# Kernel tuning notes

Measured on AMD Instinct MI355X. Metric: run time of the kernel, lower is better.

The kernel has to match this reference:

```python
import jax, jax.numpy as jnp
import numpy as np

SHARED_DIM = 512
ENC_IN = 512
LATENT = 16
BATCH = 65536
NUM_CLASSES = 16


def setup_inputs() -> dict:
    key = jax.random.key(0)
    ks = jax.random.split(key, 12)
    s = 1.0 / np.sqrt(SHARED_DIM)
    si = 1.0 / np.sqrt(ENC_IN)
    return {
        "x": jax.random.normal(ks[0], (BATCH, ENC_IN), dtype=jnp.float32),
        # shared MLP: two ReLU hiddens + identity output (rlkit Mlp)
        "W0": jax.random.uniform(ks[1], (SHARED_DIM, ENC_IN), jnp.float32, -si, si),
        "b0": jnp.zeros((SHARED_DIM,), jnp.float32),
        "W1": jax.random.uniform(ks[2], (SHARED_DIM, SHARED_DIM), jnp.float32, -s, s),
        "b1": jnp.zeros((SHARED_DIM,), jnp.float32),
        "W2": jax.random.uniform(ks[3], (SHARED_DIM, SHARED_DIM), jnp.float32, -s, s),
        "b2": jnp.zeros((SHARED_DIM,), jnp.float32),
        # class encoder (router)
        "Wc": jax.random.uniform(ks[4], (NUM_CLASSES, SHARED_DIM), jnp.float32, -s, s),
        "bc": jnp.zeros((NUM_CLASSES,), jnp.float32),
        # per-class gaussian experts, stacked: [K, 2*latent, shared_dim]
        "Wg": jax.random.uniform(ks[5], (NUM_CLASSES, 2 * LATENT, SHARED_DIM), jnp.float32, -s, s),
        "bg": jnp.zeros((NUM_CLASSES, 2 * LATENT), jnp.float32),
    }


def reference(x, W0, b0, W1, b1, W2, b2, Wc, bc, Wg, bg):
    # shared encoder: ReLU MLP with identity output layer
    m = jax.nn.relu(x @ W0.T + b0)
    m = jax.nn.relu(m @ W1.T + b1)
    m = m @ W2.T + b2                      # [B, D]
    # router: softmax over classes, then most-likely class per sample
    y_probs = jax.nn.softmax(m @ Wc.T + bc, axis=-1)   # [B, K]
    y = jnp.argmax(y_probs, axis=1)                    # [B]
    # evaluate ALL per-class experts densely (as the original does)
    mu_sigma = jnp.einsum('bd,ked->bke', m, Wg) + bg   # [B, K, 2L]
    mu = mu_sigma[..., :LATENT]                        # Normal mean; sampler='mean'
    # gather the selected class's mean per sample
    z = jnp.take_along_axis(mu, y[:, None, None], axis=1)[:, 0, :]  # [B, L]
    return (z, y)
```

## Files before the change

### kernel.cpp

```cpp
#include <hip/hip_runtime.h>
#include <hip/hip_bf16.h>

typedef __attribute__((ext_vector_type(8))) short short8;
typedef __attribute__((ext_vector_type(16))) float floatx16;
typedef __attribute__((ext_vector_type(4))) float floatx4;

#define AS1 __attribute__((address_space(1)))
#define AS3 __attribute__((address_space(3)))

constexpr int MM = 65536;
constexpr int KK = 512;
constexpr int NN = 512;

#define GK 32
#define LDT 40

__device__ __forceinline__ unsigned short bf16_rn(float v) {
  unsigned u = __float_as_uint(v);
  return (unsigned short)((u + 0x7FFFu + ((u >> 16) & 1u)) >> 16);
}
__device__ __forceinline__ float bf16_to_f32(unsigned short h) {
  return __uint_as_float((unsigned)h << 16);
}

__global__ __launch_bounds__(256) void split_kernel(
    const float* __restrict__ src, unsigned short* __restrict__ h,
    unsigned short* __restrict__ l, int n4) {
  int i = blockIdx.x * 256 + threadIdx.x;
  if (i >= n4) return;
  float4 v = ((const float4*)src)[i];
  ushort4 hv, lv;
  hv.x = bf16_rn(v.x); lv.x = bf16_rn(v.x - bf16_to_f32(hv.x));
  hv.y = bf16_rn(v.y); lv.y = bf16_rn(v.y - bf16_to_f32(hv.y));
  hv.z = bf16_rn(v.z); lv.z = bf16_rn(v.z - bf16_to_f32(hv.z));
  hv.w = bf16_rn(v.w); lv.w = bf16_rn(v.w - bf16_to_f32(hv.w));
  ((ushort4*)h)[i] = hv;
  ((ushort4*)l)[i] = lv;
}

template<bool RELU>
__global__ __launch_bounds__(512, 1) void gemm_mfma(
    const unsigned short* __restrict__ Ah, const unsigned short* __restrict__ Al,
    const unsigned short* __restrict__ Wh, const unsigned short* __restrict__ Wl,
    const float* __restrict__ bias,
    unsigned short* __restrict__ Ch, unsigned short* __restrict__ Cl) {
  __shared__ __align__(16) unsigned short smem[65536];
  const int tid = threadIdx.x;
  const int lane = tid & 63;
  const int wid = tid >> 6;
  const int wr = wid >> 2;
  const int wc = wid & 3;
  const int nwg = gridDim.x;
  const int hw  = blockIdx.x;
  const int logical = (hw & 7) * (nwg >> 3) + (hw >> 3);
  const int bm = logical >> 1, bn = logical & 1;
  const size_t Abase = (size_t)bm * 256 * KK;
  const size_t Bbase = (size_t)bn * 256 * KK;

  const int sarr  = wid >> 1;
  const int rbase = (wid & 1) * 128;
  const unsigned short* gsrc = (sarr == 0) ? Ah : (sarr == 1) ? Al
                             : (sarr == 2) ? Wh : Wl;
  const size_t tb = (sarr < 2) ? Abase : Bbase;
  const int rowl = lane >> 2;
  const int gch  = (lane & 3) ^ ((lane >> 3) & 3);
  const unsigned short* gbase = gsrc + tb + (size_t)(rbase + rowl) * KK + gch * 8;
  unsigned short* ldst = smem + sarr * 8192 + rbase * 32;

  auto stage2 = [&](int buf, int kk, int p) {
#pragma unroll
    for (int j = p * 2; j < p * 2 + 2; ++j) {
      __builtin_amdgcn_global_load_lds(
          (const AS1 unsigned int*)(gbase + (size_t)(j * 16) * KK + kk),
          (AS3 unsigned int*)(ldst + buf * 32768 + j * 16 * 32),
          16, 0, 0);
    }
  };

  floatx16 acc[4][2];
#pragma unroll
  for (int i = 0; i < 4; ++i)
#pragma unroll
    for (int j = 0; j < 2; ++j)
#pragma unroll
      for (int r = 0; r < 16; ++r) acc[i][j][r] = 0.f;

#pragma unroll
  for (int p = 0; p < 4; ++p) stage2(0, 0, p);

  const int swz = (lane >> 1) & 3;
#pragma unroll
  for (int t = 0; t < 16; ++t) {
    const int cur = t & 1;
    const unsigned short* base = smem + cur * 32768;
    short8 fbh[2], fbl[2];
#pragma unroll
    for (int p = 0; p < 4; ++p) {
      const int ks = p >> 1, h = p & 1;
      const int ch = ks * 2 + (lane >> 5);
      const int sw = (ch ^ swz) * 8;
      short8 fah[2], fal[2];

      if (p == 0) {
        if (t < 15) {
          stage2(cur ^ 1, (t + 1) * GK, 0);
          asm volatile("s_waitcnt vmcnt(2)" ::: "memory");
        } else {
          asm volatile("s_waitcnt vmcnt(0)" ::: "memory");
        }
        __builtin_amdgcn_s_barrier();
        __builtin_amdgcn_sched_barrier(0);
      }

#pragma unroll
      for (int q = 0; q < 2; ++q) {
        int row = wr * 128 + (h * 2 + q) * 32 + (lane & 31);
        fah[q] = *(const short8*)(base + row * 32 + sw);
        fal[q] = *(const short8*)(base + 8192 + row * 32 + sw);
      }
      if (h == 0) {
#pragma unroll
        for (int si = 0; si < 2; ++si) {
          int col = wc * 64 + si * 32 + (lane & 31);
          fbh[si] = *(const short8*)(base + 16384 + col * 32 + sw);
          fbl[si] = *(const short8*)(base + 24576 + col * 32 + sw);
        }
      }

      if (p > 0) {
        if (t < 15) stage2(cur ^ 1, (t + 1) * GK, p);
        __builtin_amdgcn_sched_barrier(0);
        __builtin_amdgcn_s_barrier();
        __builtin_amdgcn_sched_barrier(0);
      }

      __builtin_amdgcn_s_setprio(1);
#pragma unroll
      for (int q = 0; q < 2; ++q)
#pragma unroll
        for (int si = 0; si < 2; ++si) {
          const int ri = h * 2 + q;
          acc[ri][si] = __builtin_amdgcn_mfma_f32_32x32x16_bf16(fah[q], fbh[si], acc[ri][si], 0, 0, 0);
          acc[ri][si] = __builtin_amdgcn_mfma_f32_32x32x16_bf16(fah[q], fbl[si], acc[ri][si], 0, 0, 0);
          acc[ri][si] = __builtin_amdgcn_mfma_f32_32x32x16_bf16(fal[q], fbh[si], acc[ri][si], 0, 0, 0);
        }
      __builtin_amdgcn_s_setprio(0);
      __builtin_amdgcn_sched_barrier(0);
      __builtin_amdgcn_s_barrier();
    }
  }

  float bv[2];
#pragma unroll
  for (int si = 0; si < 2; ++si)
    bv[si] = bias[bn * 256 + wc * 64 + si * 32 + (lane & 31)];

  unsigned* lds32 = (unsigned*)smem;
#pragma unroll
  for (int ri = 0; ri < 4; ++ri) {
    __syncthreads();
#pragma unroll
    for (int si = 0; si < 2; ++si) {
      int lcol = wc * 64 + si * 32 + (lane & 31);
#pragma unroll
      for (int r = 0; r < 16; ++r) {
        int frow = (r & 3) + 8 * (r >> 2) + 4 * (lane >> 5);
        float v = acc[ri][si][r] + bv[si];
        if (RELU) v = fmaxf(v, 0.f);
        unsigned short h = bf16_rn(v);
        unsigned short lo = bf16_rn(v - bf16_to_f32(h));
        lds32[(wr * 32 + frow) * 256 + lcol] = (unsigned)h | ((unsigned)lo << 16);
      }
    }
    __syncthreads();
#pragma unroll
    for (int p = 0; p < 8; ++p) {
      int c = tid + p * 512;
      int lrow = c >> 6;
      int cc = (c & 63) * 4;
      uint4 d = *(const uint4*)&lds32[lrow * 256 + cc];
      ushort4 hv, lv;
      hv.x = (unsigned short)(d.x); lv.x = (unsigned short)(d.x >> 16);
      hv.y = (unsigned short)(d.y); lv.y = (unsigned short)(d.y >> 16);
      hv.z = (unsigned short)(d.z); lv.z = (unsigned short)(d.z >> 16);
      hv.w = (unsigned short)(d.w); lv.w = (unsigned short)(d.w >> 16);
      int grow = bm * 256 + (lrow >> 5) * 128 + ri * 32 + (lrow & 31);
      size_t gi = (size_t)grow * NN + bn * 256 + cc;
      *(ushort4*)&Ch[gi] = hv;
      *(ushort4*)&Cl[gi] = lv;
    }
  }
}

__global__ __launch_bounds__(512, 1) void gemm_x(
    const float* __restrict__ X,
    const unsigned short* __restrict__ Wh, const unsigned short* __restrict__ Wl,
    const float* __restrict__ bias,
    unsigned short* __restrict__ Ch, unsigned short* __restrict__ Cl) {
  __shared__ __align__(16) unsigned short smem[65536];
  const int tid = threadIdx.x;
  const int lane = tid & 63;
  const int wid = tid >> 6;
  const int wr = wid >> 2;
  const int wc = wid & 3;
  const int nwg = gridDim.x;
  const int hw  = blockIdx.x;
  const int logical = (hw & 7) * (nwg >> 3) + (hw >> 3);
  const int bm = logical >> 1, bn = logical & 1;

  const int barr = wid >> 2;
  const int brb  = (wid & 3) * 64;
  const int rowl = lane >> 2;
  const int gch  = (lane & 3) ^ ((lane >> 3) & 3);
  const unsigned short* gbB = (barr ? Wl : Wh) + (size_t)bn * 256 * KK
                            + (size_t)(brb + rowl) * KK + gch * 8;
  unsigned short* ldB = smem + (2 + barr) * 8192 + brb * 32;

  auto stageB = [&](int buf, int kk) {
#pragma unroll
    for (int j = 0; j < 4; ++j) {
      __builtin_amdgcn_global_load_lds(
          (const AS1 unsigned int*)(gbB + (size_t)(j * 16) * KK + kk),
          (AS3 unsigned int*)(ldB + buf * 32768 + j * 16 * 32),
          16, 0, 0);
    }
  };

  const int arow = lane >> 3;
  const int akc  = lane & 7;
  const float* gx = X + ((size_t)(bm * 256 + wid * 32) + arow) * KK + akc * 4;
  auto loadA = [&](int kk, float4* av) {
#pragma unroll
    for (int j = 0; j < 4; ++j)
      av[j] = *(const float4*)(gx + (size_t)(j * 8) * KK + kk);
  };
  const int apc = ((akc >> 1) ^ ((arow >> 1) & 3));
  const int aoff = (wid * 32 + arow) * 32 + apc * 8 + (akc & 1) * 4;
  auto writeA = [&](int buf, const float4* av) {
#pragma unroll
    for (int j = 0; j < 4; ++j) {
      ushort4 hv, lv;
      hv.x = bf16_rn(av[j].x); lv.x = bf16_rn(av[j].x - bf16_to_f32(hv.x));
      hv.y = bf16_rn(av[j].y); lv.y = bf16_rn(av[j].y - bf16_to_f32(hv.y));
      hv.z = bf16_rn(av[j].z); lv.z = bf16_rn(av[j].z - bf16_to_f32(hv.z));
      hv.w = bf16_rn(av[j].w); lv.w = bf16_rn(av[j].w - bf16_to_f32(hv.w));
      int o = buf * 32768 + aoff + j * 8 * 32;
      *(ushort4*)(smem + o) = hv;
      *(ushort4*)(smem + 8192 + o) = lv;
    }
  };

  floatx16 acc[4][2];
#pragma unroll
  for (int i = 0; i < 4; ++i)
#pragma unroll
    for (int j = 0; j < 2; ++j)
#pragma unroll
      for (int r = 0; r < 16; ++r) acc[i][j][r] = 0.f;

  {
    float4 av0[4];
    stageB(0, 0);
    loadA(0, av0);
    asm volatile("s_waitcnt vmcnt(0)" ::: "memory");
    writeA(0, av0);
    asm volatile("s_waitcnt lgkmcnt(0)" ::: "memory");
    __builtin_amdgcn_s_barrier();
  }

  const int swz = (lane >> 1) & 3;
#pragma unroll
  for (int t = 0; t < 16; ++t) {
    const int cur = t & 1;
    const unsigned short* base = smem + cur * 32768;
    short8 fbh[2], fbl[2];
    float4 av[4];
#pragma unroll
    for (int p = 0; p < 4; ++p) {
      const int ks = p >> 1, h = p & 1;
      const int ch = ks * 2 + (lane >> 5);
      const int sw = (ch ^ swz) * 8;
      short8 fah[2], fal[2];

      if (p == 0 && t < 15) {
        stageB(cur ^ 1, (t + 1) * GK);
        loadA((t + 1) * GK, av);
      }

#pragma unroll
      for (int q = 0; q < 2; ++q) {
        int row = wr * 128 + (h * 2 + q) * 32 + (lane & 31);
        fah[q] = *(const short8*)(base + row * 32 + sw);
        fal[q] = *(const short8*)(base + 8192 + row * 32 + sw);
      }
      if (h == 0) {
#pragma unroll
        for (int si = 0; si < 2; ++si) {
          int col = wc * 64 + si * 32 + (lane & 31);
          fbh[si] = *(const short8*)(base + 16384 + col * 32 + sw);
          fbl[si] = *(const short8*)(base + 24576 + col * 32 + sw);
        }
      }

      __builtin_amdgcn_s_setprio(1);
#pragma unroll
      for (int q = 0; q < 2; ++q)
#pragma unroll
        for (int si = 0; si < 2; ++si) {
          const int ri = h * 2 + q;
          acc[ri][si] = __builtin_amdgcn_mfma_f32_32x32x16_bf16(fah[q], fbh[si], acc[ri][si], 0, 0, 0);
          acc[ri][si] = __builtin_amdgcn_mfma_f32_32x32x16_bf16(fah[q], fbl[si], acc[ri][si], 0, 0, 0);
          acc[ri][si] = __builtin_amdgcn_mfma_f32_32x32x16_bf16(fal[q], fbh[si], acc[ri][si], 0, 0, 0);
        }
      __builtin_amdgcn_s_setprio(0);
      __builtin_amdgcn_sched_barrier(0);

      if (p == 3) {
        if (t < 15) {
          asm volatile("s_waitcnt vmcnt(0)" ::: "memory");
          writeA(cur ^ 1, av);
        }
        asm volatile("s_waitcnt lgkmcnt(0)" ::: "memory");
        __builtin_amdgcn_s_barrier();
      } else {
        __builtin_amdgcn_s_barrier();
      }
      __builtin_amdgcn_sched_barrier(0);
    }
  }

  float bv[2];
#pragma unroll
  for (int si = 0; si < 2; ++si)
    bv[si] = bias[bn * 256 + wc * 64 + si * 32 + (lane & 31)];

  unsigned* lds32 = (unsigned*)smem;
#pragma unroll
  for (int ri = 0; ri < 4; ++ri) {
    __syncthreads();
#pragma unroll
    for (int si = 0; si < 2; ++si) {
      int lcol = wc * 64 + si * 32 + (lane & 31);
#pragma unroll
      for (int r = 0; r < 16; ++r) {
        int frow = (r & 3) + 8 * (r >> 2) + 4 * (lane >> 5);
        float v = fmaxf(acc[ri][si][r] + bv[si], 0.f);
        unsigned short h = bf16_rn(v);
        unsigned short lo = bf16_rn(v - bf16_to_f32(h));
        lds32[(wr * 32 + frow) * 256 + lcol] = (unsigned)h | ((unsigned)lo << 16);
      }
    }
    __syncthreads();
#pragma unroll
    for (int p = 0; p < 8; ++p) {
      int c = tid + p * 512;
      int lrow = c >> 6;
      int cc = (c & 63) * 4;
      uint4 d = *(const uint4*)&lds32[lrow * 256 + cc];
      ushort4 hv, lv;
      hv.x = (unsigned short)(d.x); lv.x = (unsigned short)(d.x >> 16);
      hv.y = (unsigned short)(d.y); lv.y = (unsigned short)(d.y >> 16);
      hv.z = (unsigned short)(d.z); lv.z = (unsigned short)(d.z >> 16);
      hv.w = (unsigned short)(d.w); lv.w = (unsigned short)(d.w >> 16);
      int grow = bm * 256 + (lrow >> 5) * 128 + ri * 32 + (lrow & 31);
      size_t gi = (size_t)grow * NN + bn * 256 + cc;
      *(ushort4*)&Ch[gi] = hv;
      *(ushort4*)&Cl[gi] = lv;
    }
  }
}

__global__ __launch_bounds__(512) void gemm_muz(
    const unsigned short* __restrict__ Ahm, const unsigned short* __restrict__ Wh,
    const float* __restrict__ bias, const float* __restrict__ y_in,
    float* __restrict__ z_out) {
  __shared__ __align__(16) unsigned short smem[32768];
  const int tid = threadIdx.x;
  const int lane = tid & 63;
  const int wid = tid >> 6;
  const int wr = wid >> 2;
  const int wc = wid & 3;
  const int bm = blockIdx.x;

  const int sarr = (wid < 4) ? 0 : 1;
  const int rb   = (wid & 3) * 64;
  const unsigned short* gsrc = sarr ? Wh : (Ahm + (size_t)bm * 256 * KK);
  const int rowl = lane >> 2;
  const int gch  = (lane & 3) ^ ((lane >> 3) & 3);
  const unsigned short* gbase = gsrc + (size_t)(rb + rowl) * KK + gch * 8;
  unsigned short* ldst = smem + sarr * 8192 + rb * 32;

  auto stage1 = [&](int buf, int kk, int j) {
    __builtin_amdgcn_global_load_lds(
        (const AS1 unsigned int*)(gbase + (size_t)(j * 16) * KK + kk),
        (AS3 unsigned int*)(ldst + buf * 16384 + j * 16 * 32),
        16, 0, 0);
  };

  floatx16 acc[4][2];
#pragma unroll
  for (int i = 0; i < 4; ++i)
#pragma unroll
    for (int j = 0; j < 2; ++j)
#pragma unroll
      for (int r = 0; r < 16; ++r) acc[i][j][r] = 0.f;

#pragma unroll
  for (int j = 0; j < 4; ++j) stage1(0, 0, j);

  const int swz = (lane >> 1) & 3;
#pragma unroll
  for (int t = 0; t < 16; ++t) {
    const int cur = t & 1;
    const unsigned short* base = smem + cur * 16384;
    short8 fb[2];
#pragma unroll
    for (int p = 0; p < 4; ++p) {
      const int ks = p >> 1, h = p & 1;
      const int ch = ks * 2 + (lane >> 5);
      const int sw = (ch ^ swz) * 8;
      short8 fa[2];

      if (p == 0) {
        if (t < 15) {
          stage1(cur ^ 1, (t + 1) * GK, 0);
          asm volatile("s_waitcnt vmcnt(1)" ::: "memory");
        } else {
          asm volatile("s_waitcnt vmcnt(0)" ::: "memory");
        }
        __builtin_amdgcn_s_barrier();
        __builtin_amdgcn_sched_barrier(0);
      }

#pragma unroll
      for (int q = 0; q < 2; ++q) {
        int row = wr * 128 + (h * 2 + q) * 32 + (lane & 31);
        fa[q] = *(const short8*)(base + row * 32 + sw);
      }
      if (h == 0) {
#pragma unroll
        for (int si = 0; si < 2; ++si) {
          int col = wc * 64 + si * 32 + (lane & 31);
          fb[si] = *(const short8*)(base + 8192 + col * 32 + sw);
        }
      }

      if (p > 0) {
        if (t < 15) stage1(cur ^ 1, (t + 1) * GK, p);
        __builtin_amdgcn_sched_barrier(0);
        __builtin_amdgcn_s_barrier();
        __builtin_amdgcn_sched_barrier(0);
      }

      __builtin_amdgcn_s_setprio(1);
#pragma unroll
      for (int q = 0; q < 2; ++q)
#pragma unroll
        for (int si = 0; si < 2; ++si)
          acc[h * 2 + q][si] = __builtin_amdgcn_mfma_f32_32x32x16_bf16(fa[q], fb[si], acc[h * 2 + q][si], 0, 0, 0);
      __builtin_amdgcn_s_setprio(0);
      __builtin_amdgcn_sched_barrier(0);
      __builtin_amdgcn_s_barrier();
    }
  }

  int colv[2]; float bv[2];
#pragma unroll
  for (int si = 0; si < 2; ++si) {
    colv[si] = wc * 64 + si * 32 + (lane & 31);
    bv[si] = bias[colv[si]];
  }
#pragma unroll
  for (int ri = 0; ri < 4; ++ri)
#pragma unroll
    for (int r = 0; r < 16; ++r) {
      int row = bm * 256 + wr * 128 + ri * 32 + (r & 3) + 8 * (r >> 2) + 4 * (lane >> 5);
      int yv = (int)y_in[row];
#pragma unroll
      for (int si = 0; si < 2; ++si) {
        if ((colv[si] >> 4) == yv)
          z_out[(size_t)row * 16 + (colv[si] & 15)] = acc[ri][si][r] + bv[si];
      }
    }
}

__global__ __launch_bounds__(256) void logits_kernel(
    const unsigned short* __restrict__ mh, const unsigned short* __restrict__ ml,
    const unsigned short* __restrict__ wch, const unsigned short* __restrict__ wcl,
    const float* __restrict__ bc, float* __restrict__ y_out) {
  __shared__ unsigned short smh[64][LDT], sml[64][LDT];
  __shared__ float slog[64][17];
  const int tid = threadIdx.x;
  const int lane = tid & 63;
  const int wid = tid >> 6;
  const size_t row0 = (size_t)blockIdx.x * 64;
  const int fr = lane & 15;
  const int fq = lane >> 4;

  floatx4 acc = {0.f, 0.f, 0.f, 0.f};
  const unsigned short* bh = wch + fr * 512 + fq * 8;
  const unsigned short* bl = wcl + fr * 512 + fq * 8;

  for (int k0 = 0; k0 < 512; k0 += 32) {
    {
      int row = tid >> 2, cc = (tid & 3) * 8;
      size_t g = (row0 + row) * 512 + k0 + cc;
      *(short8*)&smh[row][cc] = *(const short8*)(mh + g);
      *(short8*)&sml[row][cc] = *(const short8*)(ml + g);
    }
    __syncthreads();
    short8 ah = *(const short8*)&smh[wid * 16 + fr][fq * 8];
    short8 al = *(const short8*)&sml[wid * 16 + fr][fq * 8];
    short8 fbh = *(const short8*)(bh + k0);
    short8 fbl = *(const short8*)(bl + k0);
    acc = __builtin_amdgcn_mfma_f32_16x16x32_bf16(ah, fbh, acc, 0, 0, 0);
    acc = __builtin_amdgcn_mfma_f32_16x16x32_bf16(ah, fbl, acc, 0, 0, 0);
    acc = __builtin_amdgcn_mfma_f32_16x16x32_bf16(al, fbh, acc, 0, 0, 0);
    __syncthreads();
  }
#pragma unroll
  for (int r = 0; r < 4; ++r)
    slog[wid * 16 + fq * 4 + r][fr] = acc[r] + bc[fr];
  __syncthreads();
  if (tid < 64) {
    float best = slog[tid][0];
    int bi = 0;
#pragma unroll
    for (int j = 1; j < 16; ++j) {
      float v = slog[tid][j];
      if (v > best) { best = v; bi = j; }
    }
    y_out[row0 + tid] = (float)bi;
  }
}

__global__ __launch_bounds__(256) void prep_wg(
    const float* __restrict__ Wg, const float* __restrict__ bg,
    unsigned short* __restrict__ wgh, float* __restrict__ wgb) {
  int gid = blockIdx.x * 256 + threadIdx.x;
  if (gid >= 32768) return;
  int r = gid >> 7;
  int c4 = (gid & 127) * 4;
  int k = r >> 4, e = r & 15;
  float4 v = *(const float4*)(Wg + ((size_t)k * 32 + e) * 512 + c4);
  ushort4 h;
  h.x = bf16_rn(v.x); h.y = bf16_rn(v.y); h.z = bf16_rn(v.z); h.w = bf16_rn(v.w);
  *(ushort4*)(wgh + (size_t)r * 512 + c4) = h;
  if (c4 == 0) wgb[r] = bg[k * 32 + e];
}

extern "C" void kernel_launch(void* const* d_in, const int* in_sizes, int n_in,
                              void* d_out, int out_size, void* d_ws, size_t ws_size,
                              hipStream_t stream) {
  const float* x  = (const float*)d_in[0];
  const float* W0 = (const float*)d_in[1];
  const float* b0 = (const float*)d_in[2];
  const float* W1 = (const float*)d_in[3];
  const float* b1 = (const float*)d_in[4];
  const float* W2 = (const float*)d_in[5];
  const float* b2 = (const float*)d_in[6];
  const float* Wc = (const float*)d_in[7];
  const float* bc = (const float*)d_in[8];
  const float* Wg = (const float*)d_in[9];
  const float* bg = (const float*)d_in[10];

  const size_t NEL = (size_t)MM * KK;
  unsigned short* Ah = (unsigned short*)d_ws;
  unsigned short* Al = Ah + NEL;
  unsigned short* Bh = Al + NEL;
  unsigned short* Bl = Bh + NEL;
  unsigned short* wch = Al;
  unsigned short* wcl = Al + 8192;
  unsigned short* wgh = Al + 16384;
  float* wgb = (float*)(Al + 16384 + 131072);

  unsigned short* w0h = (unsigned short*)d_out;
  unsigned short* w0l = w0h + 262144;
  unsigned short* w1h = w0l + 262144;
  unsigned short* w1l = w1h + 262144;
  unsigned short* w2h = w1l + 262144;
  unsigned short* w2l = w2h + 262144;

  float* z_out = (float*)d_out;
  float* y_out = z_out + (size_t)MM * 16;

  split_kernel<<<256, 256, 0, stream>>>(W0, w0h, w0l, 65536);
  split_kernel<<<256, 256, 0, stream>>>(W1, w1h, w1l, 65536);
  split_kernel<<<256, 256, 0, stream>>>(W2, w2h, w2l, 65536);

  const int ngrid = (MM / 256) * (NN / 256);
  gemm_x<<<ngrid, 512, 0, stream>>>(x, w0h, w0l, b0, Bh, Bl);
  gemm_mfma<true ><<<ngrid, 512, 0, stream>>>(Bh, Bl, w1h, w1l, b1, Ah, Al);
  gemm_mfma<false><<<ngrid, 512, 0, stream>>>(Ah, Al, w2h, w2l, b2, Bh, Bl);

  split_kernel<<<8, 256, 0, stream>>>(Wc, wch, wcl, 2048);
  prep_wg<<<128, 256, 0, stream>>>(Wg, bg, wgh, wgb);

  logits_kernel<<<MM / 64, 256, 0, stream>>>(Bh, Bl, wch, wcl, bc, y_out);
  gemm_muz<<<MM / 256, 512, 0, stream>>>(Bh, wgh, wgb, y_out, z_out);
}
```

Before: 587.0 us.

## Fuse router logits and argmax into the expert-mean GEMM kernel

Merges the separate logits/argmax kernel into the mu GEMM kernel. The fused kernel stages both hi and lo halves of m plus the Wg tile in LDS, runs the 16-class router MFMAs alongside the main MFMAs, computes the argmax in shared memory, and uses it locally to select z. This removes a second full read of the m activations (hi and lo) and one kernel launch. In exchange it uses more LDS per block (limiting occupancy to one block per CU) and adds extra loads and barriers per iteration.

Result: slower. 634.0 us (median of 2 runs) (+8.0%).

```diff
diff --git a/kernel.cpp b/kernel.cpp
--- a/kernel.cpp
+++ b/kernel.cpp
@@ -13,7 +13,6 @@
 constexpr int NN = 512;
 
 #define GK 32
-#define LDT 40
 
 __device__ __forceinline__ unsigned short bf16_rn(float v) {
   unsigned u = __float_as_uint(v);
@@ -370,49 +369,88 @@
   }
 }
 
-__global__ __launch_bounds__(512) void gemm_muz(
-    const unsigned short* __restrict__ Ahm, const unsigned short* __restrict__ Wh,
-    const float* __restrict__ bias, const float* __restrict__ y_in,
-    float* __restrict__ z_out) {
-  __shared__ __align__(16) unsigned short smem[32768];
+__global__ __launch_bounds__(512, 1) void gemm_head(
+    const unsigned short* __restrict__ mh, const unsigned short* __restrict__ ml,
+    const unsigned short* __restrict__ wgh, const float* __restrict__ wgb,
+    const unsigned short* __restrict__ wch, const unsigned short* __restrict__ wcl,
+    const float* __restrict__ bc,
+    float* __restrict__ y_out, float* __restrict__ z_out) {
+  __shared__ __align__(16) unsigned short smem[65792];
   const int tid = threadIdx.x;
   const int lane = tid & 63;
   const int wid = tid >> 6;
   const int wr = wid >> 2;
-  const int wc = wid & 3;
+  const int wcs = wid & 3;
   const int bm = blockIdx.x;
-
-  const int sarr = (wid < 4) ? 0 : 1;
-  const int rb   = (wid & 3) * 64;
-  const unsigned short* gsrc = sarr ? Wh : (Ahm + (size_t)bm * 256 * KK);
+  const int fr = lane & 15, fq = lane >> 4;
+
+  const unsigned short* baseA0 = mh + (size_t)bm * 256 * KK;
+  const unsigned short* baseA1 = ml + (size_t)bm * 256 * KK;
   const int rowl = lane >> 2;
   const int gch  = (lane & 3) ^ ((lane >> 3) & 3);
-  const unsigned short* gbase = gsrc + (size_t)(rb + rowl) * KK + gch * 8;
-  unsigned short* ldst = smem + sarr * 8192 + rb * 32;
-
-  auto stage1 = [&](int buf, int kk, int j) {
+  const unsigned short* gb[6];
+  int ldo[6];
+#pragma unroll
+  for (int i = 0; i < 6; ++i) {
+    int s = wid * 6 + i;
+    int arr = s >> 4, seg = s & 15;
+    const unsigned short* b = (arr == 0) ? baseA0 : (arr == 1) ? baseA1 : wgh;
+    gb[i] = b + (size_t)(seg * 16 + rowl) * KK + gch * 8;
+    ldo[i] = arr * 8192 + seg * 16 * 32;
+  }
+  auto stageH = [&](int buf, int kk, int i) {
     __builtin_amdgcn_global_load_lds(
-        (const AS1 unsigned int*)(gbase + (size_t)(j * 16) * KK + kk),
-        (AS3 unsigned int*)(ldst + buf * 16384 + j * 16 * 32),
+        (const AS1 unsigned int*)(gb[i] + kk),
+        (AS3 unsigned int*)(smem + buf * 24576 + ldo[i]),
         16, 0, 0);
   };
 
-  floatx16 acc[4][2];
+  const float bcv = bc[fr];
+  int colv[2]; float bvmu[2];
+#pragma unroll
+  for (int si = 0; si < 2; ++si) {
+    colv[si] = wcs * 64 + si * 32 + (lane & 31);
+    bvmu[si] = wgb[colv[si]];
+  }
+
+  {
+    short8 r0[2], r1[2];
+#pragma unroll
+    for (int q = 0; q < 2; ++q) {
+      int c = tid + q * 512;
+      int row = c >> 6, cc = (c & 63) * 8;
+      r0[q] = *(const short8*)(wch + row * 512 + cc);
+      r1[q] = *(const short8*)(wcl + row * 512 + cc);
+    }
+#pragma unroll
+    for (int q = 0; q < 2; ++q) {
+      int c = tid + q * 512;
+      int row = c >> 6, cc = (c & 63) * 8;
+      *(short8*)(smem + 49152 + row * 520 + cc) = r0[q];
+      *(short8*)(smem + 57472 + row * 520 + cc) = r1[q];
+    }
+#pragma unroll
+    for (int i = 0; i < 6; ++i) stageH(0, 0, i);
+    asm volatile("s_waitcnt vmcnt(0) lgkmcnt(0)" ::: "memory");
+    __builtin_amdgcn_s_barrier();
+  }
+
+  floatx16 accm[4][2];
 #pragma unroll
   for (int i = 0; i < 4; ++i)
 #pragma unroll
     for (int j = 0; j < 2; ++j)
 #pragma unroll
-      for (int r = 0; r < 16; ++r) acc[i][j][r] = 0.f;
-
-#pragma unroll
-  for (int j = 0; j < 4; ++j) stage1(0, 0, j);
+      for (int r = 0; r < 16; ++r) accm[i][j][r] = 0.f;
+  floatx4 accl0 = {0.f, 0.f, 0.f, 0.f};
+  floatx4 accl1 = {0.f, 0.f, 0.f, 0.f};
 
   const int swz = (lane >> 1) & 3;
+  const int lsw = (fq ^ ((fr >> 1) & 3)) * 8;
 #pragma unroll
   for (int t = 0; t < 16; ++t) {
     const int cur = t & 1;
-    const unsigned short* base = smem + cur * 16384;
+    const unsigned short* base = smem + cur * 24576;
     short8 fb[2];
 #pragma unroll
     for (int p = 0; p < 4; ++p) {
@@ -423,8 +461,9 @@
 
       if (p == 0) {
         if (t < 15) {
-          stage1(cur ^ 1, (t + 1) * GK, 0);
-          asm volatile("s_waitcnt vmcnt(1)" ::: "memory");
+          stageH(cur ^ 1, (t + 1) * GK, 0);
+          stageH(cur ^ 1, (t + 1) * GK, 1);
+          asm volatile("s_waitcnt vmcnt(2)" ::: "memory");
         } else {
           asm volatile("s_waitcnt vmcnt(0)" ::: "memory");
         }
@@ -440,13 +479,25 @@
       if (h == 0) {
 #pragma unroll
         for (int si = 0; si < 2; ++si) {
-          int col = wc * 64 + si * 32 + (lane & 31);
-          fb[si] = *(const short8*)(base + 8192 + col * 32 + sw);
-        }
+          int col = wcs * 64 + si * 32 + (lane & 31);
+          fb[si] = *(const short8*)(base + 16384 + col * 32 + sw);
+        }
+      }
+      short8 lah, lal, lbh, lbl;
+      if (p & 1) {
+        const int g = p >> 1;
+        int lrow = wid * 32 + g * 16 + fr;
+        lah = *(const short8*)(base + lrow * 32 + lsw);
+        lal = *(const short8*)(base + 8192 + lrow * 32 + lsw);
+        lbh = *(const short8*)(smem + 49152 + fr * 520 + t * 32 + fq * 8);
+        lbl = *(const short8*)(smem + 57472 + fr * 520 + t * 32 + fq * 8);
       }
 
       if (p > 0) {
-        if (t < 15) stage1(cur ^ 1, (t + 1) * GK, p);
+        if (t < 15 && p < 3) {
+          stageH(cur ^ 1, (t + 1) * GK, p * 2);
+          stageH(cur ^ 1, (t + 1) * GK, p * 2 + 1);
+        }
         __builtin_amdgcn_sched_barrier(0);
         __builtin_amdgcn_s_barrier();
         __builtin_amdgcn_sched_barrier(0);
@@ -457,81 +508,56 @@
       for (int q = 0; q < 2; ++q)
 #pragma unroll
         for (int si = 0; si < 2; ++si)
-          acc[h * 2 + q][si] = __builtin_amdgcn_mfma_f32_32x32x16_bf16(fa[q], fb[si], acc[h * 2 + q][si], 0, 0, 0);
+          accm[h * 2 + q][si] = __builtin_amdgcn_mfma_f32_32x32x16_bf16(fa[q], fb[si], accm[h * 2 + q][si], 0, 0, 0);
+      if (p == 1) {
+        accl0 = __builtin_amdgcn_mfma_f32_16x16x32_bf16(lah, lbh, accl0, 0, 0, 0);
+        accl0 = __builtin_amdgcn_mfma_f32_16x16x32_bf16(lah, lbl, accl0, 0, 0, 0);
+        accl0 = __builtin_amdgcn_mfma_f32_16x16x32_bf16(lal, lbh, accl0, 0, 0, 0);
+      }
+      if (p == 3) {
+        accl1 = __builtin_amdgcn_mfma_f32_16x16x32_bf16(lah, lbh, accl1, 0, 0, 0);
+        accl1 = __builtin_amdgcn_mfma_f32_16x16x32_bf16(lah, lbl, accl1, 0, 0, 0);
+        accl1 = __builtin_amdgcn_mfma_f32_16x16x32_bf16(lal, lbh, accl1, 0, 0, 0);
+      }
       __builtin_amdgcn_s_setprio(0);
       __builtin_amdgcn_sched_barrier(0);
       __builtin_amdgcn_s_barrier();
     }
   }
 
-  int colv[2]; float bv[2];
-#pragma unroll
-  for (int si = 0; si < 2; ++si) {
-    colv[si] = wc * 64 + si * 32 + (lane & 31);
-    bv[si] = bias[colv[si]];
-  }
+  __syncthreads();
+  float* slog = (float*)smem;
+  float* yl = slog + 256 * 17;
+#pragma unroll
+  for (int r = 0; r < 4; ++r) {
+    slog[(wid * 32 + 0 * 16 + fq * 4 + r) * 17 + fr] = accl0[r] + bcv;
+    slog[(wid * 32 + 1 * 16 + fq * 4 + r) * 17 + fr] = accl1[r] + bcv;
+  }
+  __syncthreads();
+  if (tid < 256) {
+    float best = slog[tid * 17];
+    int bi = 0;
+#pragma unroll
+    for (int j = 1; j < 16; ++j) {
+      float v = slog[tid * 17 + j];
+      if (v > best) { best = v; bi = j; }
+    }
+    yl[tid] = (float)bi;
+    y_out[(size_t)bm * 256 + tid] = (float)bi;
+  }
+  __syncthreads();
 #pragma unroll
   for (int ri = 0; ri < 4; ++ri)
 #pragma unroll
     for (int r = 0; r < 16; ++r) {
-      int row = bm * 256 + wr * 128 + ri * 32 + (r & 3) + 8 * (r >> 2) + 4 * (lane >> 5);
-      int yv = (int)y_in[row];
+      int rowL = wr * 128 + ri * 32 + (r & 3) + 8 * (r >> 2) + 4 * (lane >> 5);
+      int yv = (int)yl[rowL];
 #pragma unroll
       for (int si = 0; si < 2; ++si) {
         if ((colv[si] >> 4) == yv)
-          z_out[(size_t)row * 16 + (colv[si] & 15)] = acc[ri][si][r] + bv[si];
-      }
-    }
-}
-
-__global__ __launch_bounds__(256) void logits_kernel(
-    const unsigned short* __restrict__ mh, const unsigned short* __restrict__ ml,
-    const unsigned short* __restrict__ wch, const unsigned short* __restrict__ wcl,
-    const float* __restrict__ bc, float* __restrict__ y_out) {
-  __shared__ unsigned short smh[64][LDT], sml[64][LDT];
-  __shared__ float slog[64][17];
-  const int tid = threadIdx.x;
-  const int lane = tid & 63;
-  const int wid = tid >> 6;
-  const size_t row0 = (size_t)blockIdx.x * 64;
-  const int fr = lane & 15;
-  const int fq = lane >> 4;
-
-  floatx4 acc = {0.f, 0.f, 0.f, 0.f};
-  const unsigned short* bh = wch + fr * 512 + fq * 8;
-  const unsigned short* bl = wcl + fr * 512 + fq * 8;
-
-  for (int k0 = 0; k0 < 512; k0 += 32) {
-    {
-      int row = tid >> 2, cc = (tid & 3) * 8;
-      size_t g = (row0 + row) * 512 + k0 + cc;
-      *(short8*)&smh[row][cc] = *(const short8*)(mh + g);
-      *(short8*)&sml[row][cc] = *(const short8*)(ml + g);
-    }
-    __syncthreads();
-    short8 ah = *(const short8*)&smh[wid * 16 + fr][fq * 8];
-    short8 al = *(const short8*)&sml[wid * 16 + fr][fq * 8];
-    short8 fbh = *(const short8*)(bh + k0);
-    short8 fbl = *(const short8*)(bl + k0);
-    acc = __builtin_amdgcn_mfma_f32_16x16x32_bf16(ah, fbh, acc, 0, 0, 0);
-    acc = __builtin_amdgcn_mfma_f32_16x16x32_bf16(ah, fbl, acc, 0, 0, 0);
-    acc = __builtin_amdgcn_mfma_f32_16x16x32_bf16(al, fbh, acc, 0, 0, 0);
-    __syncthreads();
-  }
-#pragma unroll
-  for (int r = 0; r < 4; ++r)
-    slog[wid * 16 + fq * 4 + r][fr] = acc[r] + bc[fr];
-  __syncthreads();
-  if (tid < 64) {
-    float best = slog[tid][0];
-    int bi = 0;
-#pragma unroll
-    for (int j = 1; j < 16; ++j) {
-      float v = slog[tid][j];
-      if (v > best) { best = v; bi = j; }
-    }
-    y_out[row0 + tid] = (float)bi;
-  }
+          z_out[((size_t)bm * 256 + rowL) * 16 + (colv[si] & 15)] = accm[ri][si][r] + bvmu[si];
+      }
+    }
 }
 
 __global__ __launch_bounds__(256) void prep_wg(
@@ -596,6 +622,5 @@
   split_kernel<<<8, 256, 0, stream>>>(Wc, wch, wcl, 2048);
   prep_wg<<<128, 256, 0, stream>>>(Wg, bg, wgh, wgb);
 
-  logits_kernel<<<MM / 64, 256, 0, stream>>>(Bh, Bl, wch, wcl, bc, y_out);
-  gemm_muz<<<MM / 256, 512, 0, stream>>>(Bh, wgh, wgb, y_out, z_out);
-}
+  gemm_head<<<MM / 256, 512, 0, stream>>>(Bh, Bl, wgh, wgb, wch, wcl, bc, y_out, z_out);
+}
```
